# Performance work log

Hardware: AMD Instinct MI355X
Metric: run time of the kernel (lower is better)

Reference implementation:

```python
import jax, jax.numpy as jnp
import numpy as np


def gcn_conv(x, src, dst, W, b, num_nodes):
    # PyG GCNConv: add self-loops, symmetric deg^-1/2 normalization, scatter-add.
    h = x @ W                                    # [N, out]
    loops = jnp.arange(num_nodes, dtype=src.dtype)
    s = jnp.concatenate([src, loops])            # [E+N]
    d = jnp.concatenate([dst, loops])            # [E+N]
    deg = jax.ops.segment_sum(jnp.ones_like(d, dtype=h.dtype), d, num_segments=num_nodes)
    dinv = jnp.where(deg > 0, jax.lax.rsqrt(deg), 0.0)
    norm = dinv[s] * dinv[d]                     # [E+N]
    msgs = h[s] * norm[:, None]                  # gather + scale  [E+N, out]
    out = jax.ops.segment_sum(msgs, d, num_segments=num_nodes)
    return out + b


NUM_GRAPHS = 512


def setup_inputs() -> dict:
    key = jax.random.key(0)
    ks = jax.random.split(key, 12)
    N, E, F = 50000, 400000, 128
    x = jax.random.normal(ks[0], (N, F), dtype=jnp.float32)
    edge_index = jax.random.randint(ks[1], (2, E), 0, N, dtype=jnp.int64)
    batch = jnp.sort(jax.random.randint(ks[2], (N,), 0, NUM_GRAPHS, dtype=jnp.int64))
    def lin(k, fi, fo):
        return jax.random.normal(k, (fi, fo), dtype=jnp.float32) * (1.0 / np.sqrt(fi))
    return {
        "x": x, "edge_index": edge_index, "batch": batch,
        "W1": lin(ks[3], F, 512), "b1": jnp.zeros((512,), jnp.float32),
        "W2": lin(ks[4], 512, 256), "b2": jnp.zeros((256,), jnp.float32),
        "W3": lin(ks[5], 256, 128), "b3": jnp.zeros((128,), jnp.float32),
        "W4": lin(ks[6], 128, 32), "b4": jnp.zeros((32,), jnp.float32),
        "W5": lin(ks[7], 32, 10), "b5": jnp.zeros((10,), jnp.float32),
    }


def reference(x, edge_index, batch, W1, b1, W2, b2, W3, b3, W4, b4, W5, b5):
    N = x.shape[0]
    src, dst = edge_index[0], edge_index[1]
    h = gcn_conv(x, src, dst, W1, b1, N)
    h = jax.nn.leaky_relu(h, negative_slope=0.01)
    h = gcn_conv(h, src, dst, W2, b2, N)          # [N, 256]
    embs = jax.ops.segment_max(h, batch, num_segments=NUM_GRAPHS)  # [G, 256]
    z = ((h @ W3 + b3) @ W4 + b4) @ W5 + b5       # [N, 10]
    out = jax.ops.segment_max(z, batch, num_segments=NUM_GRAPHS)   # [G, 10]
    return (out, embs)
```

## Files before the change

### kernel.cpp

```cpp
#include <hip/hip_runtime.h>
#include <math.h>

#define DIV_UP(a,b) (((a)+(b)-1)/(b))

typedef __attribute__((ext_vector_type(8))) short bf16x8;
typedef __attribute__((ext_vector_type(4))) float f32x4;

__device__ inline unsigned short f2b(float x) {
    unsigned int u = __float_as_uint(x);
    u += 0x7fffu + ((u >> 16) & 1u);
    return (unsigned short)(u >> 16);
}

__device__ inline void cvt8(uint4 v, float* a) {
    a[0] = __uint_as_float(v.x << 16); a[1] = __uint_as_float(v.x & 0xffff0000u);
    a[2] = __uint_as_float(v.y << 16); a[3] = __uint_as_float(v.y & 0xffff0000u);
    a[4] = __uint_as_float(v.z << 16); a[5] = __uint_as_float(v.z & 0xffff0000u);
    a[6] = __uint_as_float(v.w << 16); a[7] = __uint_as_float(v.w & 0xffff0000u);
}

__device__ inline void atomicMaxF(float* addr, float v) {
    if (v >= 0.f) atomicMax((int*)addr, __float_as_int(v));
    else          atomicMin((unsigned int*)addr, __float_as_uint(v));
}

__device__ inline void gl16(void* lds, const void* g) {
    __builtin_amdgcn_global_load_lds(
        (const __attribute__((address_space(1))) void*)g,
        (__attribute__((address_space(3))) void*)lds, 16, 0, 0);
}

__global__ void k_zero_i(int* p, int n) {
    int i = blockIdx.x * blockDim.x + threadIdx.x;
    if (i < n) p[i] = 0;
}

__global__ void k_hist(const int* __restrict__ dst, int* __restrict__ hist, int E) {
    int i = blockIdx.x * blockDim.x + threadIdx.x;
    if (i < E) atomicAdd(&hist[dst[i]], 1);
}

__global__ __launch_bounds__(256) void k_scan_bsum(const int* __restrict__ hist,
                                                   int* __restrict__ bsum, int N) {
    __shared__ int red[256];
    int t = threadIdx.x;
    int base = blockIdx.x * 1024 + t * 4;
    int s = 0;
    if (base + 3 < N) {
        int4 v = *(const int4*)&hist[base];
        s = v.x + v.y + v.z + v.w;
    } else {
        for (int j = 0; j < 4; ++j) if (base + j < N) s += hist[base + j];
    }
    red[t] = s;
    __syncthreads();
    for (int off = 128; off >= 1; off >>= 1) {
        if (t < off) red[t] += red[t + off];
        __syncthreads();
    }
    if (t == 0) bsum[blockIdx.x] = red[0];
}

__global__ __launch_bounds__(1024) void k_scan_boff(const int* __restrict__ bsum,
        int* __restrict__ boff, int* __restrict__ row_off, int NB, int N) {
    __shared__ int s[1024];
    int t = threadIdx.x;
    int v = (t < NB) ? bsum[t] : 0;
    s[t] = v;
    __syncthreads();
    for (int off = 1; off < 1024; off <<= 1) {
        int u = (t >= off) ? s[t - off] : 0;
        __syncthreads();
        s[t] += u;
        __syncthreads();
    }
    if (t < NB) boff[t] = s[t] - v;
    if (t == NB - 1) row_off[N] = s[t];
}

__global__ __launch_bounds__(256) void k_scan_apply(const int* __restrict__ hist,
        const int* __restrict__ boff, int* __restrict__ row_off,
        float* __restrict__ dinv, int N) {
    __shared__ int s[256];
    int t = threadIdx.x;
    int base = blockIdx.x * 1024 + t * 4;
    int v[4];
    int loc = 0;
#pragma unroll
    for (int j = 0; j < 4; ++j) { v[j] = (base + j < N) ? hist[base + j] : 0; loc += v[j]; }
    s[t] = loc;
    __syncthreads();
    for (int off = 1; off < 256; off <<= 1) {
        int u = (t >= off) ? s[t - off] : 0;
        __syncthreads();
        s[t] += u;
        __syncthreads();
    }
    int run = boff[blockIdx.x] + s[t] - loc;
#pragma unroll
    for (int j = 0; j < 4; ++j) {
        if (base + j < N) {
            row_off[base + j] = run;
            dinv[base + j] = rsqrtf((float)(v[j] + 1));
        }
        run += v[j];
    }
}

__global__ void k_bin(const int* __restrict__ src, const int* __restrict__ dst,
                      const int* __restrict__ row_off, int* __restrict__ cursor,
                      const float* __restrict__ dinv,
                      int* __restrict__ csr_src, float* __restrict__ csr_w, int E) {
    int i = blockIdx.x * blockDim.x + threadIdx.x;
    if (i >= E) return;
    int d = dst[i], s = src[i];
    int pos = row_off[d] + atomicAdd(&cursor[d], 1);
    csr_src[pos] = s;
    csr_w[pos] = dinv[s] * dinv[d];
}

__global__ __launch_bounds__(256) void k_pre(
        const float* __restrict__ W3, const float* __restrict__ W4,
        const float* __restrict__ W5, const float* __restrict__ b3,
        const float* __restrict__ b4, const float* __restrict__ b5,
        float* __restrict__ WcT, float* __restrict__ bc,
        unsigned* __restrict__ outp, int nout, int nfo,
        const float* __restrict__ x, unsigned short* __restrict__ xb, int n4,
        const float* __restrict__ W1, unsigned short* __restrict__ w1t, int K1, int N1,
        const float* __restrict__ W2, unsigned short* __restrict__ w2t, int K2, int N2) {
    int b = blockIdx.x;
    int t = threadIdx.x;
    if (b < 11) {
        int c = b;
        if (c < 10) {
            __shared__ float Tc[128];
            if (t < 128) {
                float s = 0.f;
#pragma unroll 8
                for (int k = 0; k < 32; ++k) s = fmaf(W4[t * 32 + k], W5[k * 10 + c], s);
                Tc[t] = s;
            }
            __syncthreads();
            float s = 0.f;
            const float* w3r = &W3[t * 128];
#pragma unroll 8
            for (int j = 0; j < 128; ++j) s = fmaf(w3r[j], Tc[j], s);
            WcT[c * 256 + t] = s;
        } else {
            __shared__ float v[32];
            if (t < 32) {
                float s = b4[t];
                for (int j = 0; j < 128; ++j) s = fmaf(b3[j], W4[j * 32 + t], s);
                v[t] = s;
            }
            __syncthreads();
            if (t < 10) {
                float s = b5[t];
                for (int k = 0; k < 32; ++k) s = fmaf(v[k], W5[k * 10 + t], s);
                bc[t] = s;
            }
        }
        return;
    }
    if (b < 11 + nfo) {
        int i = (b - 11) * 256 + t;
        if (i < nout) outp[i] = 0xff800000u;
        return;
    }
    int i = (b - 11 - nfo) * 256 + t;
    if (i < n4) {
        float4 v = ((const float4*)x)[i];
        ushort4 o;
        o.x = f2b(v.x); o.y = f2b(v.y); o.z = f2b(v.z); o.w = f2b(v.w);
        ((ushort4*)xb)[i] = o;
        return;
    }
    i -= n4;
    if (i < K1 * N1) {
        int k = i / N1, n = i % N1;
        w1t[(size_t)n * K1 + k] = f2b(W1[i]);
        return;
    }
    i -= K1 * N1;
    if (i < K2 * N2) {
        int k = i / N2, n = i % N2;
        w2t[(size_t)n * K2 + k] = f2b(W2[i]);
    }
}

template <int F>
__global__ __launch_bounds__(256) void k_gather_b(const unsigned short* __restrict__ H,
        const int* __restrict__ row_off, const int* __restrict__ csr_src,
        const float* __restrict__ csr_w, const float* __restrict__ dinv,
        const float* __restrict__ bias, unsigned short* __restrict__ outb, int N) {
    const int LPN = F / 8;
    const int NPB = 256 / LPN;
    int node = blockIdx.x * NPB + threadIdx.x / LPN;
    if (node >= N) return;
    int f = (threadIdx.x % LPN) * 8;
    const unsigned short* Hf = H + f;
    float sc = dinv[node]; sc *= sc;
    float a[8];
    cvt8(*(const uint4*)&Hf[(size_t)node * F], a);
#pragma unroll
    for (int j = 0; j < 8; ++j) a[j] *= sc;
    if (bias) {
#pragma unroll
        for (int j = 0; j < 8; ++j) a[j] += bias[f + j];
    }
    int e0 = row_off[node], e1 = row_off[node + 1];
    int ee = e1 - 1;
    for (int e = e0; e < e1; e += 6) {
        int i0 = e;
        int i1 = min(e + 1, ee), i2 = min(e + 2, ee), i3 = min(e + 3, ee);
        int i4 = min(e + 4, ee), i5 = min(e + 5, ee);
        int s0 = csr_src[i0], s1 = csr_src[i1], s2 = csr_src[i2];
        int s3 = csr_src[i3], s4 = csr_src[i4], s5 = csr_src[i5];
        float w0 = csr_w[i0];
        float w1 = (e + 1 <= ee) ? csr_w[i1] : 0.f;
        float w2 = (e + 2 <= ee) ? csr_w[i2] : 0.f;
        float w3 = (e + 3 <= ee) ? csr_w[i3] : 0.f;
        float w4 = (e + 4 <= ee) ? csr_w[i4] : 0.f;
        float w5 = (e + 5 <= ee) ? csr_w[i5] : 0.f;
        uint4 v0 = *(const uint4*)&Hf[(size_t)s0 * F];
        uint4 v1 = *(const uint4*)&Hf[(size_t)s1 * F];
        uint4 v2 = *(const uint4*)&Hf[(size_t)s2 * F];
        uint4 v3 = *(const uint4*)&Hf[(size_t)s3 * F];
        uint4 v4 = *(const uint4*)&Hf[(size_t)s4 * F];
        uint4 v5 = *(const uint4*)&Hf[(size_t)s5 * F];
        float bb[8];
        cvt8(v0, bb);
#pragma unroll
        for (int j = 0; j < 8; ++j) a[j] = fmaf(w0, bb[j], a[j]);
        cvt8(v1, bb);
#pragma unroll
        for (int j = 0; j < 8; ++j) a[j] = fmaf(w1, bb[j], a[j]);
        cvt8(v2, bb);
#pragma unroll
        for (int j = 0; j < 8; ++j) a[j] = fmaf(w2, bb[j], a[j]);
        cvt8(v3, bb);
#pragma unroll
        for (int j = 0; j < 8; ++j) a[j] = fmaf(w3, bb[j], a[j]);
        cvt8(v4, bb);
#pragma unroll
        for (int j = 0; j < 8; ++j) a[j] = fmaf(w4, bb[j], a[j]);
        cvt8(v5, bb);
#pragma unroll
        for (int j = 0; j < 8; ++j) a[j] = fmaf(w5, bb[j], a[j]);
    }
    uint4 o;
    o.x = (unsigned)f2b(a[0]) | ((unsigned)f2b(a[1]) << 16);
    o.y = (unsigned)f2b(a[2]) | ((unsigned)f2b(a[3]) << 16);
    o.z = (unsigned)f2b(a[4]) | ((unsigned)f2b(a[5]) << 16);
    o.w = (unsigned)f2b(a[6]) | ((unsigned)f2b(a[7]) << 16);
    *(uint4*)&outb[(size_t)node * F + f] = o;
}

__global__ __launch_bounds__(256) void k_gather_head(
        const unsigned short* __restrict__ H,
        const int* __restrict__ row_off, const int* __restrict__ csr_src,
        const float* __restrict__ csr_w, const float* __restrict__ dinv,
        const float* __restrict__ bias, const int* __restrict__ batch,
        const float* __restrict__ WcT, const float* __restrict__ bc,
        float* __restrict__ out, float* __restrict__ out_emb, int N) {
    __shared__ __align__(16) float Ws[10][260];
    __shared__ float bs[10];
    __shared__ __align__(16) float h2s[8][264];
    __shared__ float zl[8][10];
    __shared__ int gl[8];
    int t = threadIdx.x;
    for (int i = t; i < 2560; i += 256) Ws[i >> 8][i & 255] = WcT[i];
    if (t < 10) bs[t] = bc[t];
    int nl = t >> 5;
    int q  = t & 31;
    int node = blockIdx.x * 8 + nl;
    bool valid = node < N;
    if (q == 0) gl[nl] = valid ? batch[node] : -1;
    int f = q * 8;
    const unsigned short* Hf = H + f;
    float a[8] = {0.f, 0.f, 0.f, 0.f, 0.f, 0.f, 0.f, 0.f};
    if (valid) {
        float sc = dinv[node]; sc *= sc;
        cvt8(*(const uint4*)&Hf[(size_t)node * 256], a);
#pragma unroll
        for (int j = 0; j < 8; ++j) a[j] = fmaf(a[j], sc, bias[f + j]);
        int e0 = row_off[node], e1 = row_off[node + 1];
        int ee = e1 - 1;
        for (int e = e0; e < e1; e += 6) {
            int i0 = e;
            int i1 = min(e + 1, ee), i2 = min(e + 2, ee), i3 = min(e + 3, ee);
            int i4 = min(e + 4, ee), i5 = min(e + 5, ee);
            int s0 = csr_src[i0], s1 = csr_src[i1], s2 = csr_src[i2];
            int s3 = csr_src[i3], s4 = csr_src[i4], s5 = csr_src[i5];
            float w0 = csr_w[i0];
            float w1 = (e + 1 <= ee) ? csr_w[i1] : 0.f;
            float w2 = (e + 2 <= ee) ? csr_w[i2] : 0.f;
            float w3 = (e + 3 <= ee) ? csr_w[i3] : 0.f;
            float w4 = (e + 4 <= ee) ? csr_w[i4] : 0.f;
            float w5 = (e + 5 <= ee) ? csr_w[i5] : 0.f;
            uint4 v0 = *(const uint4*)&Hf[(size_t)s0 * 256];
            uint4 v1 = *(const uint4*)&Hf[(size_t)s1 * 256];
            uint4 v2 = *(const uint4*)&Hf[(size_t)s2 * 256];
            uint4 v3 = *(const uint4*)&Hf[(size_t)s3 * 256];
            uint4 v4 = *(const uint4*)&Hf[(size_t)s4 * 256];
            uint4 v5 = *(const uint4*)&Hf[(size_t)s5 * 256];
            float bb[8];
            cvt8(v0, bb);
#pragma unroll
            for (int j = 0; j < 8; ++j) a[j] = fmaf(w0, bb[j], a[j]);
            cvt8(v1, bb);
#pragma unroll
            for (int j = 0; j < 8; ++j) a[j] = fmaf(w1, bb[j], a[j]);
            cvt8(v2, bb);
#pragma unroll
            for (int j = 0; j < 8; ++j) a[j] = fmaf(w2, bb[j], a[j]);
            cvt8(v3, bb);
#pragma unroll
            for (int j = 0; j < 8; ++j) a[j] = fmaf(w3, bb[j], a[j]);
            cvt8(v4, bb);
#pragma unroll
            for (int j = 0; j < 8; ++j) a[j] = fmaf(w4, bb[j], a[j]);
            cvt8(v5, bb);
#pragma unroll
            for (int j = 0; j < 8; ++j) a[j] = fmaf(w5, bb[j], a[j]);
        }
    }
    __syncthreads();

#pragma unroll
    for (int c = 0; c < 10; ++c) {
        float4 wa = *(const float4*)&Ws[c][f];
        float4 wb = *(const float4*)&Ws[c][f + 4];
        float s = a[0] * wa.x;
        s = fmaf(a[1], wa.y, s);
        s = fmaf(a[2], wa.z, s);
        s = fmaf(a[3], wa.w, s);
        s = fmaf(a[4], wb.x, s);
        s = fmaf(a[5], wb.y, s);
        s = fmaf(a[6], wb.z, s);
        s = fmaf(a[7], wb.w, s);
        s += __shfl_xor(s, 16);
        s += __shfl_xor(s, 8);
        s += __shfl_xor(s, 4);
        s += __shfl_xor(s, 2);
        s += __shfl_xor(s, 1);
        if (q == 0) zl[nl][c] = s + bs[c];
    }
    *(float4*)&h2s[nl][f]     = make_float4(a[0], a[1], a[2], a[3]);
    *(float4*)&h2s[nl][f + 4] = make_float4(a[4], a[5], a[6], a[7]);
    __syncthreads();

    {
        int curg = -1; float m = 0.f;
#pragma unroll
        for (int n = 0; n < 8; ++n) {
            int g = gl[n];
            if (g < 0) continue;
            float v = h2s[n][t];
            if (g != curg) {
                if (curg >= 0) atomicMaxF(&out_emb[(size_t)curg * 256 + t], m);
                curg = g; m = v;
            } else {
                m = fmaxf(m, v);
            }
        }
        if (curg >= 0) atomicMaxF(&out_emb[(size_t)curg * 256 + t], m);
    }
    if (t < 10) {
        int curg = -1; float m = 0.f;
#pragma unroll
        for (int n = 0; n < 8; ++n) {
            int g = gl[n];
            if (g < 0) continue;
            float v = zl[n][t];
            if (g != curg) {
                if (curg >= 0) atomicMaxF(&out[(size_t)curg * 10 + t], m);
                curg = g; m = v;
            } else {
                m = fmaxf(m, v);
            }
        }
        if (curg >= 0) atomicMaxF(&out[(size_t)curg * 10 + t], m);
    }
}

template <int OUT_BF16, int ACT>
__global__ __launch_bounds__(512) void k_gemm_mfma256(const unsigned short* __restrict__ A,
        const unsigned short* __restrict__ Bt, const float* __restrict__ bias,
        void* __restrict__ Cout, int M, int K, int NC) {
    __shared__ __align__(16) unsigned short As[128][64];
    __shared__ __align__(16) unsigned short Bs[256][64];
    int tid = threadIdx.x;
    int wave = tid >> 6, lane = tid & 63;
    int row0 = blockIdx.y * 128, col0 = blockIdx.x * 256;
    int wr = (wave >> 2) * 64, wc = (wave & 3) * 64;
    f32x4 acc[4][4] = {};
    int lr = lane & 15;
    int lg = lane >> 4;
    int sw = ((lane & 7) ^ (lane >> 3)) << 3;
    int ch0 = (lg ^ (lr & 7)) << 3;
    int ch1 = ch0 ^ (4 << 3);

    for (int k0 = 0; k0 < K; k0 += 64) {
#pragma unroll
        for (int c = 0; c < 2; ++c) {
            int rl = c * 64 + wave * 8 + (lane >> 3);
            int gr = min(row0 + rl, M - 1);
            gl16(&As[c * 64 + wave * 8][0], &A[(size_t)gr * K + k0 + sw]);
        }
#pragma unroll
        for (int c = 0; c < 4; ++c) {
            int rl = c * 64 + wave * 8 + (lane >> 3);
            gl16(&Bs[c * 64 + wave * 8][0], &Bt[(size_t)(col0 + rl) * K + k0 + sw]);
        }
        __syncthreads();
        bf16x8 af[2][4], bv[2][4];
#pragma unroll
        for (int i = 0; i < 4; ++i) {
            int ra = wr + i * 16 + lr;
            int rb = wc + i * 16 + lr;
            af[0][i] = *(const bf16x8*)&As[ra][ch0];
            af[1][i] = *(const bf16x8*)&As[ra][ch1];
            bv[0][i] = *(const bf16x8*)&Bs[rb][ch0];
            bv[1][i] = *(const bf16x8*)&Bs[rb][ch1];
        }
#pragma unroll
        for (int s = 0; s < 2; ++s)
#pragma unroll
            for (int i = 0; i < 4; ++i)
#pragma unroll
                for (int j = 0; j < 4; ++j)
                    acc[i][j] = __builtin_amdgcn_mfma_f32_16x16x32_bf16(bv[s][j], af[s][i], acc[i][j], 0, 0, 0);
        __syncthreads();
    }

    int q4 = lg * 4;
    float4 bb[4];
#pragma unroll
    for (int j = 0; j < 4; ++j)
        bb[j] = bias ? *(const float4*)&bias[col0 + wc + j * 16 + q4]
                     : make_float4(0.f, 0.f, 0.f, 0.f);
#pragma unroll
    for (int i = 0; i < 4; ++i) {
        int row = row0 + wr + i * 16 + lr;
        if (row >= M) continue;
#pragma unroll
        for (int j = 0; j < 4; ++j) {
            int c0 = col0 + wc + j * 16 + q4;
            float4 v;
            v.x = acc[i][j][0] + bb[j].x;
            v.y = acc[i][j][1] + bb[j].y;
            v.z = acc[i][j][2] + bb[j].z;
            v.w = acc[i][j][3] + bb[j].w;
            if (ACT) {
                v.x = (v.x >= 0.f) ? v.x : 0.01f * v.x;
                v.y = (v.y >= 0.f) ? v.y : 0.01f * v.y;
                v.z = (v.z >= 0.f) ? v.z : 0.01f * v.z;
                v.w = (v.w >= 0.f) ? v.w : 0.01f * v.w;
            }
            if (OUT_BF16) {
                uint2 o;
                o.x = (unsigned)f2b(v.x) | ((unsigned)f2b(v.y) << 16);
                o.y = (unsigned)f2b(v.z) | ((unsigned)f2b(v.w) << 16);
                *(uint2*)&((unsigned short*)Cout)[(size_t)row * NC + c0] = o;
            } else {
                *(float4*)&((float*)Cout)[(size_t)row * NC + c0] = v;
            }
        }
    }
}

extern "C" void kernel_launch(void* const* d_in, const int* in_sizes, int n_in,
                              void* d_out, int out_size, void* d_ws, size_t ws_size,
                              hipStream_t stream) {
    const float* x  = (const float*)d_in[0];
    const int* ei   = (const int*)d_in[1];
    const int* batch= (const int*)d_in[2];
    const float* W1 = (const float*)d_in[3];
    const float* b1 = (const float*)d_in[4];
    const float* W2 = (const float*)d_in[5];
    const float* b2 = (const float*)d_in[6];
    const float* W3 = (const float*)d_in[7];
    const float* b3 = (const float*)d_in[8];
    const float* W4 = (const float*)d_in[9];
    const float* b4 = (const float*)d_in[10];
    const float* W5 = (const float*)d_in[11];
    const float* b5 = (const float*)d_in[12];

    const int N  = in_sizes[2];
    const int F  = in_sizes[0] / N;
    const int E  = in_sizes[1] / 2;
    const int C1 = in_sizes[4];
    const int C2 = in_sizes[6];
    const int C5 = in_sizes[12];
    const int G  = out_size / (C2 + C5);
    const int NB = DIV_UP(N, 1024);

    const int* srcp = ei;
    const int* dstp = ei + E;

    uintptr_t p = (uintptr_t)d_ws;
    auto carve = [&](size_t bytes) {
        uintptr_t r = p;
        p += (bytes + 255) & ~(size_t)255;
        return (void*)r;
    };
    int* hist    = (int*)carve(sizeof(int) * N);
    int* cursor  = (int*)carve(sizeof(int) * N);
    int* row_off = (int*)carve(sizeof(int) * (N + 1));
    int* bsum    = (int*)carve(sizeof(int) * NB);
    int* boff    = (int*)carve(sizeof(int) * NB);
    int* csr_src = (int*)carve(sizeof(int) * E);
    float* csr_w = (float*)carve(sizeof(float) * E);
    float* dinv  = (float*)carve(sizeof(float) * N);
    float* wct   = (float*)carve(sizeof(float) * C2 * C5);
    float* bcv   = (float*)carve(sizeof(float) * C5);
    unsigned short* w1t = (unsigned short*)carve(sizeof(short) * F * C1);
    unsigned short* w2t = (unsigned short*)carve(sizeof(short) * C1 * C2);
    unsigned short* xb    = (unsigned short*)carve(sizeof(short) * (size_t)N * F);
    unsigned short* aggxb = (unsigned short*)carve(sizeof(short) * (size_t)N * F);
    unsigned short* h1b   = (unsigned short*)carve(sizeof(short) * (size_t)N * C1);
    unsigned short* t2b   = (unsigned short*)carve(sizeof(short) * (size_t)N * C2);

    float* out     = (float*)d_out;
    float* out_emb = out + (size_t)G * C5;

    int zspan = (int)(((sizeof(int) * N + 255) & ~(size_t)255) / 4) + N;
    k_zero_i<<<DIV_UP(zspan, 256), 256, 0, stream>>>(hist, zspan);
    k_hist<<<DIV_UP(E, 256), 256, 0, stream>>>(dstp, hist, E);
    k_scan_bsum<<<NB, 256, 0, stream>>>(hist, bsum, N);
    k_scan_boff<<<1, 1024, 0, stream>>>(bsum, boff, row_off, NB, N);
    k_scan_apply<<<NB, 256, 0, stream>>>(hist, boff, row_off, dinv, N);
    k_bin<<<DIV_UP(E, 256), 256, 0, stream>>>(srcp, dstp, row_off, cursor, dinv,
                                              csr_src, csr_w, E);

    int n4 = N * F / 4;
    int nout = G * (C2 + C5);
    int nfo = DIV_UP(nout, 256);
    int prep_total = n4 + F * C1 + C1 * C2;
    int pre_blocks = 11 + nfo + DIV_UP(prep_total, 256);
    k_pre<<<pre_blocks, 256, 0, stream>>>(W3, W4, W5, b3, b4, b5, wct, bcv,
                                          (unsigned*)d_out, nout, nfo,
                                          x, xb, n4, W1, w1t, F, C1, W2, w2t, C1, C2);

    k_gather_b<128><<<DIV_UP(N, 16), 256, 0, stream>>>(
        xb, row_off, csr_src, csr_w, dinv, nullptr, aggxb, N);
    dim3 g1(C1 / 256, DIV_UP(N, 128));
    k_gemm_mfma256<1, 1><<<g1, 512, 0, stream>>>(aggxb, w1t, b1, h1b, N, F, C1);

    dim3 g2(C2 / 256, DIV_UP(N, 128));
    k_gemm_mfma256<1, 0><<<g2, 512, 0, stream>>>(h1b, w2t, nullptr, t2b, N, C1, C2);

    k_gather_head<<<DIV_UP(N, 8), 256, 0, stream>>>(
        t2b, row_off, csr_src, csr_w, dinv, b2, batch, wct, bcv,
        out, out_emb, N);
}
```

Measured before the change: 271.8 us.

## Software-pipeline edge gathers in head kernel via LDS-staged neighbor lists

Each 32-lane node group now stages up to 32 neighbor indices and weights in LDS. A new rotating-register pipeline then keeps two batches of four row loads in flight while the previous batch is accumulated, with any remaining edges handled by a scalar loop. The per-block LDS copy of the 10x256 classifier weights and the __syncthreads after the gather are removed, and those weights are read directly from global memory instead. This is meant to raise memory-level parallelism and cut LDS footprint and setup work, at the cost of more registers and a wave-local LDS dependency with no explicit barrier.

```diff
diff --git a/kernel.cpp b/kernel.cpp
--- a/kernel.cpp
+++ b/kernel.cpp
@@ -28,6 +28,93 @@
     __builtin_amdgcn_global_load_lds(
         (const __attribute__((address_space(1))) void*)g,
         (__attribute__((address_space(3))) void*)lds, 16, 0, 0);
+}
+
+template <int F>
+__device__ inline void edge_accum2(const unsigned short* __restrict__ Hf,
+        const int* __restrict__ sI, const float* __restrict__ sW,
+        int cap, float* a) {
+    if (cap <= 0) return;
+    int cm = cap - 1;
+    uint4 A0, A1, A2, A3, B0, B1, B2, B3;
+    {
+        int s0 = sI[0],           s1 = sI[min(1, cm)];
+        int s2 = sI[min(2, cm)],  s3 = sI[min(3, cm)];
+        A0 = *(const uint4*)&Hf[(size_t)s0 * F];
+        A1 = *(const uint4*)&Hf[(size_t)s1 * F];
+        A2 = *(const uint4*)&Hf[(size_t)s2 * F];
+        A3 = *(const uint4*)&Hf[(size_t)s3 * F];
+        int t0 = sI[min(4, cm)],  t1 = sI[min(5, cm)];
+        int t2 = sI[min(6, cm)],  t3 = sI[min(7, cm)];
+        B0 = *(const uint4*)&Hf[(size_t)t0 * F];
+        B1 = *(const uint4*)&Hf[(size_t)t1 * F];
+        B2 = *(const uint4*)&Hf[(size_t)t2 * F];
+        B3 = *(const uint4*)&Hf[(size_t)t3 * F];
+    }
+    int k = 0;
+    float bb[8];
+    while (k + 8 < cap) {
+        int u0 = sI[min(k + 8, cm)],  u1 = sI[min(k + 9, cm)];
+        int u2 = sI[min(k + 10, cm)], u3 = sI[min(k + 11, cm)];
+        uint4 C0 = *(const uint4*)&Hf[(size_t)u0 * F];
+        uint4 C1 = *(const uint4*)&Hf[(size_t)u1 * F];
+        uint4 C2 = *(const uint4*)&Hf[(size_t)u2 * F];
+        uint4 C3 = *(const uint4*)&Hf[(size_t)u3 * F];
+        __builtin_amdgcn_sched_barrier(0);
+        float w0 = sW[k], w1 = sW[k + 1], w2 = sW[k + 2], w3 = sW[k + 3];
+        cvt8(A0, bb);
+#pragma unroll
+        for (int j = 0; j < 8; ++j) a[j] = fmaf(w0, bb[j], a[j]);
+        cvt8(A1, bb);
+#pragma unroll
+        for (int j = 0; j < 8; ++j) a[j] = fmaf(w1, bb[j], a[j]);
+        cvt8(A2, bb);
+#pragma unroll
+        for (int j = 0; j < 8; ++j) a[j] = fmaf(w2, bb[j], a[j]);
+        cvt8(A3, bb);
+#pragma unroll
+        for (int j = 0; j < 8; ++j) a[j] = fmaf(w3, bb[j], a[j]);
+        A0 = B0; A1 = B1; A2 = B2; A3 = B3;
+        B0 = C0; B1 = C1; B2 = C2; B3 = C3;
+        k += 4;
+    }
+    {
+        float w0 = sW[k];
+        float w1 = (k + 1 <= cm) ? sW[k + 1] : 0.f;
+        float w2 = (k + 2 <= cm) ? sW[k + 2] : 0.f;
+        float w3 = (k + 3 <= cm) ? sW[k + 3] : 0.f;
+        cvt8(A0, bb);
+#pragma unroll
+        for (int j = 0; j < 8; ++j) a[j] = fmaf(w0, bb[j], a[j]);
+        cvt8(A1, bb);
+#pragma unroll
+        for (int j = 0; j < 8; ++j) a[j] = fmaf(w1, bb[j], a[j]);
+        cvt8(A2, bb);
+#pragma unroll
+        for (int j = 0; j < 8; ++j) a[j] = fmaf(w2, bb[j], a[j]);
+        cvt8(A3, bb);
+#pragma unroll
+        for (int j = 0; j < 8; ++j) a[j] = fmaf(w3, bb[j], a[j]);
+    }
+    k += 4;
+    if (k <= cm) {
+        float w0 = sW[k];
+        float w1 = (k + 1 <= cm) ? sW[k + 1] : 0.f;
+        float w2 = (k + 2 <= cm) ? sW[k + 2] : 0.f;
+        float w3 = (k + 3 <= cm) ? sW[k + 3] : 0.f;
+        cvt8(B0, bb);
+#pragma unroll
+        for (int j = 0; j < 8; ++j) a[j] = fmaf(w0, bb[j], a[j]);
+        cvt8(B1, bb);
+#pragma unroll
+        for (int j = 0; j < 8; ++j) a[j] = fmaf(w1, bb[j], a[j]);
+        cvt8(B2, bb);
+#pragma unroll
+        for (int j = 0; j < 8; ++j) a[j] = fmaf(w2, bb[j], a[j]);
+        cvt8(B3, bb);
+#pragma unroll
+        for (int j = 0; j < 8; ++j) a[j] = fmaf(w3, bb[j], a[j]);
+    }
 }
 
 __global__ void k_zero_i(int* p, int n) {
@@ -263,14 +350,12 @@
         const float* __restrict__ bias, const int* __restrict__ batch,
         const float* __restrict__ WcT, const float* __restrict__ bc,
         float* __restrict__ out, float* __restrict__ out_emb, int N) {
-    __shared__ __align__(16) float Ws[10][260];
-    __shared__ float bs[10];
     __shared__ __align__(16) float h2s[8][264];
     __shared__ float zl[8][10];
     __shared__ int gl[8];
+    __shared__ int   sIdx[8][32];
+    __shared__ float sWt[8][32];
     int t = threadIdx.x;
-    for (int i = t; i < 2560; i += 256) Ws[i >> 8][i & 255] = WcT[i];
-    if (t < 10) bs[t] = bc[t];
     int nl = t >> 5;
     int q  = t & 31;
     int node = blockIdx.x * 8 + nl;
@@ -285,52 +370,26 @@
 #pragma unroll
         for (int j = 0; j < 8; ++j) a[j] = fmaf(a[j], sc, bias[f + j]);
         int e0 = row_off[node], e1 = row_off[node + 1];
-        int ee = e1 - 1;
-        for (int e = e0; e < e1; e += 6) {
-            int i0 = e;
-            int i1 = min(e + 1, ee), i2 = min(e + 2, ee), i3 = min(e + 3, ee);
-            int i4 = min(e + 4, ee), i5 = min(e + 5, ee);
-            int s0 = csr_src[i0], s1 = csr_src[i1], s2 = csr_src[i2];
-            int s3 = csr_src[i3], s4 = csr_src[i4], s5 = csr_src[i5];
-            float w0 = csr_w[i0];
-            float w1 = (e + 1 <= ee) ? csr_w[i1] : 0.f;
-            float w2 = (e + 2 <= ee) ? csr_w[i2] : 0.f;
-            float w3 = (e + 3 <= ee) ? csr_w[i3] : 0.f;
-            float w4 = (e + 4 <= ee) ? csr_w[i4] : 0.f;
-            float w5 = (e + 5 <= ee) ? csr_w[i5] : 0.f;
-            uint4 v0 = *(const uint4*)&Hf[(size_t)s0 * 256];
-            uint4 v1 = *(const uint4*)&Hf[(size_t)s1 * 256];
-            uint4 v2 = *(const uint4*)&Hf[(size_t)s2 * 256];
-            uint4 v3 = *(const uint4*)&Hf[(size_t)s3 * 256];
-            uint4 v4 = *(const uint4*)&Hf[(size_t)s4 * 256];
-            uint4 v5 = *(const uint4*)&Hf[(size_t)s5 * 256];
-            float bb[8];
-            cvt8(v0, bb);
-#pragma unroll
-            for (int j = 0; j < 8; ++j) a[j] = fmaf(w0, bb[j], a[j]);
-            cvt8(v1, bb);
-#pragma unroll
-            for (int j = 0; j < 8; ++j) a[j] = fmaf(w1, bb[j], a[j]);
-            cvt8(v2, bb);
-#pragma unroll
-            for (int j = 0; j < 8; ++j) a[j] = fmaf(w2, bb[j], a[j]);
-            cvt8(v3, bb);
-#pragma unroll
-            for (int j = 0; j < 8; ++j) a[j] = fmaf(w3, bb[j], a[j]);
-            cvt8(v4, bb);
-#pragma unroll
-            for (int j = 0; j < 8; ++j) a[j] = fmaf(w4, bb[j], a[j]);
-            cvt8(v5, bb);
-#pragma unroll
-            for (int j = 0; j < 8; ++j) a[j] = fmaf(w5, bb[j], a[j]);
-        }
-    }
-    __syncthreads();
+        int deg = e1 - e0;
+        int cap = min(deg, 32);
+        if (q < cap) { sIdx[nl][q] = csr_src[e0 + q]; sWt[nl][q] = csr_w[e0 + q]; }
+        edge_accum2<256>(Hf, &sIdx[nl][0], &sWt[nl][0], cap, a);
+        if (deg > 32) {
+            for (int e = e0 + 32; e < e1; ++e) {
+                int s = csr_src[e];
+                float w = csr_w[e];
+                float bb[8];
+                cvt8(*(const uint4*)&Hf[(size_t)s * 256], bb);
+#pragma unroll
+                for (int j = 0; j < 8; ++j) a[j] = fmaf(w, bb[j], a[j]);
+            }
+        }
+    }
 
 #pragma unroll
     for (int c = 0; c < 10; ++c) {
-        float4 wa = *(const float4*)&Ws[c][f];
-        float4 wb = *(const float4*)&Ws[c][f + 4];
+        float4 wa = *(const float4*)&WcT[c * 256 + f];
+        float4 wb = *(const float4*)&WcT[c * 256 + f + 4];
         float s = a[0] * wa.x;
         s = fmaf(a[1], wa.y, s);
         s = fmaf(a[2], wa.z, s);
@@ -344,7 +403,7 @@
         s += __shfl_xor(s, 4);
         s += __shfl_xor(s, 2);
         s += __shfl_xor(s, 1);
-        if (q == 0) zl[nl][c] = s + bs[c];
+        if (q == 0) zl[nl][c] = s + bc[c];
     }
     *(float4*)&h2s[nl][f]     = make_float4(a[0], a[1], a[2], a[3]);
     *(float4*)&h2s[nl][f + 4] = make_float4(a[4], a[5], a[6], a[7]);
```

Result: slower. 283.6 us (+4.3%).
